# Optimization experiments

Hardware: AMD Instinct MI355X
Metric: run time of the kernel (lower is better)

Reference implementation:

```python
import jax, jax.numpy as jnp
import numpy as np

NUM_LEVEL = 16
LOG_T = 19
TABLE_SIZE = 2 ** LOG_T
FEAT = 2
MIN_RES = 16
MAX_RES = 512
N_POINTS = 262144

# [Teschner et al. 2003] spatial hash primes, wrapped to int32 like torch does
HASH_COEFFS = jnp.asarray(np.array([1, 2654435761, 805459861], dtype=np.uint32).astype(np.int32))


def _resolutions():
    coeff = (MAX_RES / MIN_RES) ** (1.0 / (NUM_LEVEL - 1))
    return jnp.floor(MIN_RES * (jnp.float32(coeff) ** jnp.arange(NUM_LEVEL, dtype=jnp.float32)))


def _spatial_hash(verts_i32):
    # verts_i32: (..., 3) int32; wrap-around int32 multiply then xor, then mod T (non-negative)
    x = HASH_COEFFS * verts_i32
    idx = jnp.bitwise_xor(jnp.bitwise_xor(x[..., 0], x[..., 1]), x[..., 2])
    return jnp.mod(idx, TABLE_SIZE)


def _hash_encode(coords, tables):
    # coords: (N,3) f32 in [0,1); tables: (L,T,F) f16
    res = _resolutions()                                   # (L,)
    scaled = coords[None, :, :] * res[:, None, None]        # (L,N,3)
    floor = jnp.floor(scaled)
    ceil = jnp.ceil(scaled)
    # 8 voxel corners via floor/ceil selection bits
    offs = jnp.asarray(np.array([[(o >> 2) & 1, (o >> 1) & 1, o & 1] for o in range(8)], dtype=np.bool_))
    sel = offs[:, None, None, :]                            # (8,1,1,3)
    corner = jnp.where(sel, ceil[None], floor[None])        # (8,L,N,3)
    comp = jnp.where(sel, floor[None], ceil[None])          # opposite corner (8,L,N,3)
    idx = _spatial_hash(corner.astype(jnp.int32))           # (8,L,N)
    # gather per-level features: tables[l][idx[:,l,:]] -> (L,8,N,F)
    feats = jax.vmap(lambda tab, i: tab[i], in_axes=(0, 1))(tables, idx)
    # trilinear weight of corner o = prod |opposite_corner - scaled|
    w = jnp.prod(jnp.abs(comp - scaled[None]), axis=-1)     # (8,L,N)
    w = jnp.transpose(w, (1, 0, 2))                         # (L,8,N)
    lvl = jnp.sum(feats.astype(jnp.float32) * w[..., None], axis=1)  # (L,N,F)
    return jnp.transpose(lvl, (1, 0, 2)).reshape(coords.shape[0], NUM_LEVEL * FEAT)


def _mlp(x, w_in, b_in, w_h0, b_h0, w_h1, b_h1, w_out, b_out):
    h = jax.nn.relu(x @ w_in.T + b_in)
    h = jax.nn.relu(h @ w_h0.T + b_h0)
    h = jax.nn.relu(h @ w_h1.T + b_h1)
    return h @ w_out.T + b_out


def setup_inputs() -> dict:
    key = jax.random.key(0)
    ks = jax.random.split(key, 8)
    coords = jax.random.uniform(ks[0], (N_POINTS, 3), dtype=jnp.float32)
    tables = (2e-4 * jax.random.uniform(ks[1], (NUM_LEVEL, TABLE_SIZE, FEAT), dtype=jnp.float32) - 1e-4).astype(jnp.float16)
    def lin(k, out_d, in_d):
        return jax.random.normal(k, (out_d, in_d), dtype=jnp.float32) * (1.0 / np.sqrt(in_d))
    return {
        'coords': coords, 'tables': tables,
        'w_in': lin(ks[2], 64, 32), 'b_in': jnp.zeros((64,), jnp.float32),
        'w_h0': lin(ks[3], 64, 64), 'b_h0': jnp.zeros((64,), jnp.float32),
        'w_h1': lin(ks[4], 64, 64), 'b_h1': jnp.zeros((64,), jnp.float32),
        'w_out': lin(ks[5], 16, 64), 'b_out': jnp.zeros((16,), jnp.float32),
    }


def reference(coords, tables, w_in, b_in, w_h0, b_h0, w_h1, b_h1, w_out, b_out):
    enc = _hash_encode(coords, tables)  # (N, 32)
    return _mlp(enc, w_in, b_in, w_h0, b_h0, w_h1, b_h1, w_out, b_out)  # (N, 16)
```

## Files before the change

### kernel.cpp

```cpp
#include <hip/hip_runtime.h>

#define NLVL 16
#define LOGT 19
#define TMASK ((1u << LOGT) - 1u)
#define SCALE 4096.0f
#define INV_SCALE (1.0f / 4096.0f)
#define NFRAG 22

typedef _Float16 half_t;
typedef half_t half8 __attribute__((ext_vector_type(8)));
typedef half_t half4 __attribute__((ext_vector_type(4)));
typedef half_t half2v __attribute__((ext_vector_type(2)));
typedef float  float4v __attribute__((ext_vector_type(4)));
typedef unsigned int uint4v __attribute__((ext_vector_type(4)));

__device__ __constant__ float RES_C[NLVL] = {16.f, 20.f, 25.f, 32.f, 40.f, 50.f, 64.f, 80.f,
                                             101.f, 128.f, 161.f, 203.f, 256.f, 322.f, 406.f, 512.f};

__device__ __forceinline__ float4v mfma16(half8 a, half8 b, float4v c) {
    return __builtin_amdgcn_mfma_f32_16x16x32_f16(a, b, c, 0, 0, 0);
}

__global__ __launch_bounds__(256, 8) void nerf_encode_w(
    const float* __restrict__ coords,
    const float2* __restrict__ tab,
    const float* __restrict__ w_in, const float* __restrict__ w_h0,
    const float* __restrict__ w_h1, const float* __restrict__ w_out,
    half8* __restrict__ frags,
    half_t* __restrict__ encT, int npts)
{
    const int bpl  = npts >> 8;
    const int nEnc = bpl * NLVL;
    const int b    = blockIdx.x;

    if (b >= nEnc) {
        if (threadIdx.x < 64) {
            const int frag = b - nEnc;
            const int lane = threadIdx.x;
            const int m    = lane & 15;
            const int quad = lane >> 4;
            const float* W; int ncol, row, col;
            if (frag < 4)       { W = w_in;  ncol = 32; row = frag * 16 + m;      col = quad * 8; }
            else if (frag < 12) { const int f = frag - 4;
                                  W = w_h0;  ncol = 64; row = (f >> 1) * 16 + m;  col = (f & 1) * 32 + quad * 8; }
            else if (frag < 20) { const int f = frag - 12;
                                  W = w_h1;  ncol = 64; row = (f >> 1) * 16 + m;  col = (f & 1) * 32 + quad * 8; }
            else                { const int f = frag - 20;
                                  W = w_out; ncol = 64; row = m;                  col = f * 32 + quad * 8; }
            const float* p = W + row * ncol + col;
            half8 r;
            #pragma unroll
            for (int j = 0; j < 8; ++j) r[j] = (half_t)p[j];
            frags[frag * 64 + lane] = r;
        }
        return;
    }

    const int half = bpl * 8;
    const int hi   = (b >= half) ? 1 : 0;
    const int l    = (b & 7) + (hi << 3);
    const int pb   = (hi ? (b - half) : b) >> 3;

    const int side = threadIdx.x & 1;
    const int base = pb * 256 + (threadIdx.x >> 1);
    const int p0 = base, p1 = base + 128;

    const float r = RES_C[l];
    const float2* __restrict__ bp = tab + (((unsigned)l) << LOGT);

    const float ax = coords[p0 * 3 + 0] * r, ay = coords[p0 * 3 + 1] * r, az = coords[p0 * 3 + 2] * r;
    const float afx = floorf(ax), afy = floorf(ay), afz = floorf(az);
    const float agx = ceilf(ax),  agy = ceilf(ay),  agz = ceilf(az);
    const unsigned ahx = side ? (unsigned)(int)agx : (unsigned)(int)afx;
    const float    awx = side ? (ax - afx) : (agx - ax);
    const unsigned ahfy = (unsigned)(int)afy * 2654435761u;
    const unsigned ahgy = (unsigned)(int)agy * 2654435761u;
    const unsigned ahfz = (unsigned)(int)afz * 805459861u;
    const unsigned ahgz = (unsigned)(int)agz * 805459861u;
    const float aty = ay - afy, atz = az - afz, auy = agy - ay, auz = agz - az;

    const float bx = coords[p1 * 3 + 0] * r, by = coords[p1 * 3 + 1] * r, bz = coords[p1 * 3 + 2] * r;
    const float bfx = floorf(bx), bfy = floorf(by), bfz = floorf(bz);
    const float bgx = ceilf(bx),  bgy = ceilf(by),  bgz = ceilf(bz);
    const unsigned bhx = side ? (unsigned)(int)bgx : (unsigned)(int)bfx;
    const float    bwx = side ? (bx - bfx) : (bgx - bx);
    const unsigned bhfy = (unsigned)(int)bfy * 2654435761u;
    const unsigned bhgy = (unsigned)(int)bgy * 2654435761u;
    const unsigned bhfz = (unsigned)(int)bfz * 805459861u;
    const unsigned bhgz = (unsigned)(int)bgz * 805459861u;
    const float bty = by - bfy, btz = bz - bfz, buy = bgy - by, buz = bgz - bz;

    const float2 a0 = bp[(ahx ^ ahfy ^ ahfz) & TMASK];
    const float2 a1 = bp[(ahx ^ ahfy ^ ahgz) & TMASK];
    const float2 a2 = bp[(ahx ^ ahgy ^ ahfz) & TMASK];
    const float2 a3 = bp[(ahx ^ ahgy ^ ahgz) & TMASK];
    const float2 b0 = bp[(bhx ^ bhfy ^ bhfz) & TMASK];
    const float2 b1 = bp[(bhx ^ bhfy ^ bhgz) & TMASK];
    const float2 b2 = bp[(bhx ^ bhgy ^ bhfz) & TMASK];
    const float2 b3 = bp[(bhx ^ bhgy ^ bhgz) & TMASK];

    const float aw0 = awx * auy * auz, aw1 = awx * auy * atz;
    const float aw2 = awx * aty * auz, aw3 = awx * aty * atz;
    const float bw0 = bwx * buy * buz, bw1 = bwx * buy * btz;
    const float bw2 = bwx * bty * buz, bw3 = bwx * bty * btz;

    float ae0 = aw0 * a0.x + aw1 * a1.x + aw2 * a2.x + aw3 * a3.x;
    float ae1 = aw0 * a0.y + aw1 * a1.y + aw2 * a2.y + aw3 * a3.y;
    float be0 = bw0 * b0.x + bw1 * b1.x + bw2 * b2.x + bw3 * b3.x;
    float be1 = bw0 * b0.y + bw1 * b1.y + bw2 * b2.y + bw3 * b3.y;

    ae0 += __shfl_xor(ae0, 1, 64);
    ae1 += __shfl_xor(ae1, 1, 64);
    be0 += __shfl_xor(be0, 1, 64);
    be1 += __shfl_xor(be1, 1, 64);

    if (side == 0) {
        half2v h0; h0[0] = (half_t)(ae0 * SCALE); h0[1] = (half_t)(ae1 * SCALE);
        half2v h1; h1[0] = (half_t)(be0 * SCALE); h1[1] = (half_t)(be1 * SCALE);
        *reinterpret_cast<half2v*>(&encT[((size_t)l * npts + p0) * 2]) = h0;
        *reinterpret_cast<half2v*>(&encT[((size_t)l * npts + p1) * 2]) = h1;
    }
}

__device__ __forceinline__ unsigned pack_relu2(float x, float y) {
    half2v h;
    h[0] = (half_t)fmaxf(x, 0.f);
    h[1] = (half_t)fmaxf(y, 0.f);
    return __builtin_bit_cast(unsigned, h);
}

__device__ __forceinline__ void xpose_relu(const float4v acc[4], int lane,
                                           half8& b0, half8& b1) {
    unsigned X[4], Y[4];
    X[0] = pack_relu2(acc[0][0], acc[0][1]);
    X[1] = pack_relu2(acc[0][2], acc[0][3]);
    X[2] = pack_relu2(acc[2][0], acc[2][1]);
    X[3] = pack_relu2(acc[2][2], acc[2][3]);
    Y[0] = pack_relu2(acc[1][0], acc[1][1]);
    Y[1] = pack_relu2(acc[1][2], acc[1][3]);
    Y[2] = pack_relu2(acc[3][0], acc[3][1]);
    Y[3] = pack_relu2(acc[3][2], acc[3][3]);
    const bool lo = (lane & 32) == 0;
    const bool ev = (lane & 16) == 0;
    uint4v u0, u1;
    #pragma unroll
    for (int j = 0; j < 4; ++j) {
        const unsigned s1 = lo ? Y[j] : X[j];
        const unsigned t1 = __shfl_xor(s1, 32, 64);
        const unsigned A1 = lo ? X[j] : t1;
        const unsigned B1 = lo ? t1 : Y[j];
        const unsigned s2 = ev ? B1 : A1;
        const unsigned t2 = __shfl_xor(s2, 16, 64);
        const unsigned a2 = ev ? A1 : t2;
        const unsigned b2 = ev ? t2 : B1;
        if (j < 2) { u0[j] = a2; u0[2 + j] = b2; }
        else       { u1[j - 2] = a2; u1[j] = b2; }
    }
    b0 = __builtin_bit_cast(half8, u0);
    b1 = __builtin_bit_cast(half8, u1);
}

__global__ __launch_bounds__(256, 3) void nerf_mlp7(
    const half_t* __restrict__ encT,
    const half8* __restrict__ frags,
    const float* __restrict__ b_in, const float* __restrict__ b_h0,
    const float* __restrict__ b_h1, const float* __restrict__ b_out,
    float* __restrict__ out, int npts)
{
    const int t    = threadIdx.x;
    const int lane = t & 63;
    const int wv   = t >> 6;
    const int m    = lane & 15;
    const int quad = lane >> 4;
    const size_t pbase = (size_t)blockIdx.x * 256 + (size_t)wv * 64;

    half8 be[4];
    #pragma unroll
    for (int T = 0; T < 4; ++T) {
        #pragma unroll
        for (int d = 0; d < 4; ++d) {
            const int L = quad * 4 + d;
            const half2v v = *reinterpret_cast<const half2v*>(
                &encT[((size_t)L * npts + pbase + T * 16 + m) * 2]);
            be[T][d * 2 + 0] = v[0];
            be[T][d * 2 + 1] = v[1];
        }
    }

    half8 bf0[4], bf1[4];

    {
        half8 w[4];
        #pragma unroll
        for (int f = 0; f < 4; ++f) w[f] = frags[(0 + f) * 64 + lane];
        float4v cin[4];
        #pragma unroll
        for (int mt = 0; mt < 4; ++mt)
            cin[mt] = (*reinterpret_cast<const float4v*>(b_in + mt * 16 + quad * 4)) * SCALE;
        #pragma unroll
        for (int T = 0; T < 4; ++T) {
            float4v acc[4];
            #pragma unroll
            for (int mt = 0; mt < 4; ++mt) acc[mt] = mfma16(w[mt], be[T], cin[mt]);
            xpose_relu(acc, lane, bf0[T], bf1[T]);
        }
    }
    {
        half8 w[8];
        #pragma unroll
        for (int f = 0; f < 8; ++f) w[f] = frags[(4 + f) * 64 + lane];
        float4v cin[4];
        #pragma unroll
        for (int mt = 0; mt < 4; ++mt)
            cin[mt] = (*reinterpret_cast<const float4v*>(b_h0 + mt * 16 + quad * 4)) * SCALE;
        #pragma unroll
        for (int T = 0; T < 4; ++T) {
            float4v acc[4];
            #pragma unroll
            for (int mt = 0; mt < 4; ++mt) {
                acc[mt] = mfma16(w[mt * 2 + 0], bf0[T], cin[mt]);
                acc[mt] = mfma16(w[mt * 2 + 1], bf1[T], acc[mt]);
            }
            xpose_relu(acc, lane, bf0[T], bf1[T]);
        }
    }
    {
        half8 w[8];
        #pragma unroll
        for (int f = 0; f < 8; ++f) w[f] = frags[(12 + f) * 64 + lane];
        float4v cin[4];
        #pragma unroll
        for (int mt = 0; mt < 4; ++mt)
            cin[mt] = (*reinterpret_cast<const float4v*>(b_h1 + mt * 16 + quad * 4)) * SCALE;
        #pragma unroll
        for (int T = 0; T < 4; ++T) {
            float4v acc[4];
            #pragma unroll
            for (int mt = 0; mt < 4; ++mt) {
                acc[mt] = mfma16(w[mt * 2 + 0], bf0[T], cin[mt]);
                acc[mt] = mfma16(w[mt * 2 + 1], bf1[T], acc[mt]);
            }
            xpose_relu(acc, lane, bf0[T], bf1[T]);
        }
    }
    {
        const half8 w0 = frags[20 * 64 + lane];
        const half8 w1 = frags[21 * 64 + lane];
        const float4v b4 = *reinterpret_cast<const float4v*>(b_out + quad * 4);
        const float4v zero = {0.f, 0.f, 0.f, 0.f};
        #pragma unroll
        for (int T = 0; T < 4; ++T) {
            float4v acc = mfma16(w0, bf0[T], zero);
            acc         = mfma16(w1, bf1[T], acc);
            float4v res;
            #pragma unroll
            for (int r = 0; r < 4; ++r) res[r] = fmaf(acc[r], INV_SCALE, b4[r]);
            *reinterpret_cast<float4v*>(out + (pbase + T * 16 + m) * 16 + quad * 4) = res;
        }
    }
}

__global__ __launch_bounds__(256, 2) void nerf_fused(
    const float* __restrict__ coords,
    const float2* __restrict__ tab,
    const float* __restrict__ w_in, const float* __restrict__ b_in,
    const float* __restrict__ w_h0, const float* __restrict__ b_h0,
    const float* __restrict__ w_h1, const float* __restrict__ b_h1,
    const float* __restrict__ w_out, const float* __restrict__ b_out,
    float* __restrict__ out, int npts)
{
    __shared__ half_t encS[256 * 40];
    __shared__ half_t actS[4][2][32 * 64];

    const int t    = threadIdx.x;
    const int lane = t & 63;
    const int wv   = t >> 6;
    const int m    = lane & 15;
    const int quad = lane >> 4;
    const int pt = blockIdx.x * 256 + t;

    {
        const float cx = coords[pt * 3 + 0];
        const float cy = coords[pt * 3 + 1];
        const float cz = coords[pt * 3 + 2];
        float enc[32];
        #pragma unroll
        for (int l = 0; l < NLVL; ++l) {
            const float r = RES_C[l];
            const float sx = cx * r, sy = cy * r, sz = cz * r;
            const float fx = floorf(sx), fy = floorf(sy), fz = floorf(sz);
            const float gx = ceilf(sx),  gy = ceilf(sy),  gz = ceilf(sz);
            const unsigned hfx = (unsigned)(int)fx;
            const unsigned hgx = (unsigned)(int)gx;
            const unsigned hfy = (unsigned)(int)fy * 2654435761u;
            const unsigned hgy = (unsigned)(int)gy * 2654435761u;
            const unsigned hfz = (unsigned)(int)fz * 805459861u;
            const unsigned hgz = (unsigned)(int)gz * 805459861u;
            const float tx = sx - fx, ty = sy - fy, tz = sz - fz;
            const float ux = gx - sx, uy = gy - sy, uz = gz - sz;
            const unsigned lbase = ((unsigned)l) << LOGT;
            float e0 = 0.f, e1 = 0.f;
            #pragma unroll
            for (int o = 0; o < 8; ++o) {
                const unsigned h = ((o & 4) ? hgx : hfx)
                                 ^ ((o & 2) ? hgy : hfy)
                                 ^ ((o & 1) ? hgz : hfz);
                const unsigned idx = h & TMASK;
                const float w = (((o & 4) ? tx : ux)
                              *  ((o & 2) ? ty : uy))
                              *  ((o & 1) ? tz : uz);
                const float2 fv = tab[lbase + idx];
                e0 = fmaf(w, fv.x, e0);
                e1 = fmaf(w, fv.y, e1);
            }
            enc[2 * l + 0] = e0;
            enc[2 * l + 1] = e1;
        }
        #pragma unroll
        for (int c = 0; c < 4; ++c) {
            half8 h8;
            #pragma unroll
            for (int j = 0; j < 8; ++j) h8[j] = (half_t)(enc[c * 8 + j] * SCALE);
            *reinterpret_cast<half8*>(&encS[t * 40 + c * 8]) = h8;
        }
    }

    auto loadA = [&](const float* __restrict__ W, int ncol, int row, int col) -> half8 {
        const float* p = W + row * ncol + col;
        const float4v lo = *reinterpret_cast<const float4v*>(p);
        const float4v hi = *reinterpret_cast<const float4v*>(p + 4);
        half8 r;
        r[0] = (half_t)lo[0]; r[1] = (half_t)lo[1]; r[2] = (half_t)lo[2]; r[3] = (half_t)lo[3];
        r[4] = (half_t)hi[0]; r[5] = (half_t)hi[1]; r[6] = (half_t)hi[2]; r[7] = (half_t)hi[3];
        return r;
    };

    half8 aL1[4], aL2[8], aL3[8], aL4[2];
    #pragma unroll
    for (int mt = 0; mt < 4; ++mt) aL1[mt] = loadA(w_in, 32, mt * 16 + m, quad * 8);
    #pragma unroll
    for (int mt = 0; mt < 4; ++mt) {
        aL2[mt * 2 + 0] = loadA(w_h0, 64, mt * 16 + m, 0 * 32 + quad * 8);
        aL2[mt * 2 + 1] = loadA(w_h0, 64, mt * 16 + m, 1 * 32 + quad * 8);
        aL3[mt * 2 + 0] = loadA(w_h1, 64, mt * 16 + m, 0 * 32 + quad * 8);
        aL3[mt * 2 + 1] = loadA(w_h1, 64, mt * 16 + m, 1 * 32 + quad * 8);
    }
    aL4[0] = loadA(w_out, 64, m, 0 * 32 + quad * 8);
    aL4[1] = loadA(w_out, 64, m, 1 * 32 + quad * 8);

    float4v bL1[4], bL2[4], bL3[4], bL4;
    #pragma unroll
    for (int mt = 0; mt < 4; ++mt) {
        bL1[mt] = *reinterpret_cast<const float4v*>(b_in + mt * 16 + quad * 4);
        bL2[mt] = *reinterpret_cast<const float4v*>(b_h0 + mt * 16 + quad * 4);
        bL3[mt] = *reinterpret_cast<const float4v*>(b_h1 + mt * 16 + quad * 4);
    }
    bL4 = *reinterpret_cast<const float4v*>(b_out + quad * 4);

    half_t* const ping = &actS[wv][0][0];
    half_t* const pong = &actS[wv][1][0];
    const float4v zero = {0.f, 0.f, 0.f, 0.f};

    auto storeTile = [&](half_t* buf, int lp, int mt, float4v acc, float4v bias) {
        half4 h4;
        #pragma unroll
        for (int r = 0; r < 4; ++r)
            h4[r] = (half_t)fmaxf(fmaf(bias[r], SCALE, acc[r]), 0.f);
        const int c16  = mt * 2 + (quad >> 1);
        const int phys = c16 ^ (lp & 7);
        *reinterpret_cast<half4*>(&buf[lp * 64 + phys * 8 + (quad & 1) * 4]) = h4;
    };
    auto loadB = [&](half_t* buf, int lp, int h) -> half8 {
        const int phys = (h * 4 + quad) ^ (lp & 7);
        return *reinterpret_cast<const half8*>(&buf[lp * 64 + phys * 8]);
    };

    for (int g = 0; g < 2; ++g) {
        #pragma unroll
        for (int nt = 0; nt < 2; ++nt) {
            const int lp   = nt * 16 + m;
            const int prow = wv * 64 + g * 32 + lp;
            const half8 bfr = *reinterpret_cast<const half8*>(&encS[prow * 40 + quad * 8]);
            #pragma unroll
            for (int mt = 0; mt < 4; ++mt) {
                float4v acc = mfma16(aL1[mt], bfr, zero);
                storeTile(ping, lp, mt, acc, bL1[mt]);
            }
            {
                const half8 p0 = loadB(ping, lp, 0);
                const half8 p1 = loadB(ping, lp, 1);
                #pragma unroll
                for (int mt = 0; mt < 4; ++mt) {
                    float4v acc = mfma16(aL2[mt * 2 + 0], p0, zero);
                    acc         = mfma16(aL2[mt * 2 + 1], p1, acc);
                    storeTile(pong, lp, mt, acc, bL2[mt]);
                }
            }
            {
                const half8 p0 = loadB(pong, lp, 0);
                const half8 p1 = loadB(pong, lp, 1);
                #pragma unroll
                for (int mt = 0; mt < 4; ++mt) {
                    float4v acc = mfma16(aL3[mt * 2 + 0], p0, zero);
                    acc         = mfma16(aL3[mt * 2 + 1], p1, acc);
                    storeTile(ping, lp, mt, acc, bL3[mt]);
                }
            }
            {
                const half8 p0 = loadB(ping, lp, 0);
                const half8 p1 = loadB(ping, lp, 1);
                float4v acc = mfma16(aL4[0], p0, zero);
                acc         = mfma16(aL4[1], p1, acc);
                float4v res;
                #pragma unroll
                for (int r = 0; r < 4; ++r)
                    res[r] = fmaf(acc[r], INV_SCALE, bL4[r]);
                const size_t ptg = (size_t)blockIdx.x * 256 + (size_t)wv * 64 + g * 32 + lp;
                *reinterpret_cast<float4v*>(out + ptg * 16 + quad * 4) = res;
            }
        }
    }
}

extern "C" void kernel_launch(void* const* d_in, const int* in_sizes, int n_in,
                              void* d_out, int out_size, void* d_ws, size_t ws_size,
                              hipStream_t stream) {
    const float*  coords = (const float*)d_in[0];
    const float2* tables = (const float2*)d_in[1];
    const float*  w_in   = (const float*)d_in[2];
    const float*  b_in   = (const float*)d_in[3];
    const float*  w_h0   = (const float*)d_in[4];
    const float*  b_h0   = (const float*)d_in[5];
    const float*  w_h1   = (const float*)d_in[6];
    const float*  b_h1   = (const float*)d_in[7];
    const float*  w_out  = (const float*)d_in[8];
    const float*  b_out  = (const float*)d_in[9];
    float* out = (float*)d_out;

    const int npts = in_sizes[0] / 3;
    const size_t encBytes  = (size_t)npts * 32 * sizeof(half_t);
    const size_t fragBytes = (size_t)NFRAG * 64 * sizeof(half8);

    if (ws_size >= encBytes + fragBytes && (npts & 255) == 0) {
        half_t* encT  = (half_t*)d_ws;
        half8*  frags = (half8*)((char*)d_ws + encBytes);
        const int bpl = npts >> 8;
        nerf_encode_w<<<bpl * NLVL + NFRAG, 256, 0, stream>>>(
            coords, tables, w_in, w_h0, w_h1, w_out, frags, encT, npts);
        nerf_mlp7<<<npts / 256, 256, 0, stream>>>(encT, frags,
                                                  b_in, b_h0, b_h1, b_out,
                                                  out, npts);
    } else {
        nerf_fused<<<npts / 256, 256, 0, stream>>>(coords, tables,
                                                   w_in, b_in, w_h0, b_h0,
                                                   w_h1, b_h1, w_out, b_out,
                                                   out, npts);
    }
}
```

Before: 197.7 us.

## Precompute compact hash grids for coarse levels and gather from LDS

For the four coarsest levels (resolutions 16 to 32), the dense (r+1)^3 grid of hashed table entries is precomputed into a compact workspace array. A new kernel stages each level's grid into shared memory (about 140 KB) and does the trilinear lookups from LDS, skipping the hash and the random global gathers. The hash-encode kernel now handles only the 12 finer levels, with a remapped block order. This adds a third kernel launch, needs one-block-per-CU occupancy for the staging kernel, and the fast path is gated on the exact test point count.

```diff
diff --git a/kernel.cpp b/kernel.cpp
--- a/kernel.cpp
+++ b/kernel.cpp
@@ -7,6 +7,11 @@
 #define INV_SCALE (1.0f / 4096.0f)
 #define NFRAG 22
 
+#define NCG 4
+#define CG_TOTAL 67687
+#define CG_TOTAL_PAD 67700
+#define CG_BLOCKS 265
+
 typedef _Float16 half_t;
 typedef half_t half8 __attribute__((ext_vector_type(8)));
 typedef half_t half4 __attribute__((ext_vector_type(4)));
@@ -16,50 +21,79 @@
 
 __device__ __constant__ float RES_C[NLVL] = {16.f, 20.f, 25.f, 32.f, 40.f, 50.f, 64.f, 80.f,
                                              101.f, 128.f, 161.f, 203.f, 256.f, 322.f, 406.f, 512.f};
+__device__ __constant__ int CG_SIZE[NCG] = {4913, 9261, 17576, 35937};
+__device__ __constant__ int CG_OFF[NCG]  = {0, 4916, 14180, 31760};
+__device__ __constant__ int CG_R1[NCG]   = {17, 21, 26, 33};
 
 __device__ __forceinline__ float4v mfma16(half8 a, half8 b, float4v c) {
     return __builtin_amdgcn_mfma_f32_16x16x32_f16(a, b, c, 0, 0, 0);
 }
 
-__global__ __launch_bounds__(256, 8) void nerf_encode_w(
+__global__ __launch_bounds__(256, 8) void nerf_encode_h12(
     const float* __restrict__ coords,
     const float2* __restrict__ tab,
     const float* __restrict__ w_in, const float* __restrict__ w_h0,
     const float* __restrict__ w_h1, const float* __restrict__ w_out,
     half8* __restrict__ frags,
+    unsigned* __restrict__ compact,
     half_t* __restrict__ encT, int npts)
 {
-    const int bpl  = npts >> 8;
-    const int nEnc = bpl * NLVL;
-    const int b    = blockIdx.x;
-
-    if (b >= nEnc) {
-        if (threadIdx.x < 64) {
-            const int frag = b - nEnc;
-            const int lane = threadIdx.x;
-            const int m    = lane & 15;
-            const int quad = lane >> 4;
-            const float* W; int ncol, row, col;
-            if (frag < 4)       { W = w_in;  ncol = 32; row = frag * 16 + m;      col = quad * 8; }
-            else if (frag < 12) { const int f = frag - 4;
-                                  W = w_h0;  ncol = 64; row = (f >> 1) * 16 + m;  col = (f & 1) * 32 + quad * 8; }
-            else if (frag < 20) { const int f = frag - 12;
-                                  W = w_h1;  ncol = 64; row = (f >> 1) * 16 + m;  col = (f & 1) * 32 + quad * 8; }
-            else                { const int f = frag - 20;
-                                  W = w_out; ncol = 64; row = m;                  col = f * 32 + quad * 8; }
-            const float* p = W + row * ncol + col;
-            half8 r;
-            #pragma unroll
-            for (int j = 0; j < 8; ++j) r[j] = (half_t)p[j];
-            frags[frag * 64 + lane] = r;
+    const int bpl   = npts >> 8;
+    const int nHash = 12 * bpl;
+    const int b     = blockIdx.x;
+
+    if (b >= nHash) {
+        const int tb = b - nHash;
+        if (tb < NFRAG) {
+            if (threadIdx.x < 64) {
+                const int frag = tb;
+                const int lane = threadIdx.x;
+                const int m    = lane & 15;
+                const int quad = lane >> 4;
+                const float* W; int ncol, row, col;
+                if (frag < 4)       { W = w_in;  ncol = 32; row = frag * 16 + m;      col = quad * 8; }
+                else if (frag < 12) { const int f = frag - 4;
+                                      W = w_h0;  ncol = 64; row = (f >> 1) * 16 + m;  col = (f & 1) * 32 + quad * 8; }
+                else if (frag < 20) { const int f = frag - 12;
+                                      W = w_h1;  ncol = 64; row = (f >> 1) * 16 + m;  col = (f & 1) * 32 + quad * 8; }
+                else                { const int f = frag - 20;
+                                      W = w_out; ncol = 64; row = m;                  col = f * 32 + quad * 8; }
+                const float* p = W + row * ncol + col;
+                half8 r;
+                #pragma unroll
+                for (int j = 0; j < 8; ++j) r[j] = (half_t)p[j];
+                frags[frag * 64 + lane] = r;
+            }
+        } else {
+            const int vid = (tb - NFRAG) * 256 + (int)threadIdx.x;
+            if (vid < CG_TOTAL) {
+                const int l = (vid >= 31750) ? 3 : (vid >= 14174) ? 2 : (vid >= 4913) ? 1 : 0;
+                const int voff = (l == 3) ? 31750 : (l == 2) ? 14174 : (l == 1) ? 4913 : 0;
+                const int v  = vid - voff;
+                const int r1 = CG_R1[l];
+                const int z  = v % r1;
+                const int r2 = v / r1;
+                const int y  = r2 % r1;
+                const int x  = r2 / r1;
+                const unsigned idx = ((unsigned)x
+                                    ^ ((unsigned)y * 2654435761u)
+                                    ^ ((unsigned)z * 805459861u)) & TMASK;
+                const float2 tv = tab[(((unsigned)l) << LOGT) + idx];
+                half2v h; h[0] = (half_t)tv.x; h[1] = (half_t)tv.y;
+                compact[CG_OFF[l] + v] = __builtin_bit_cast(unsigned, h);
+            }
         }
         return;
     }
 
-    const int half = bpl * 8;
-    const int hi   = (b >= half) ? 1 : 0;
-    const int l    = (b & 7) + (hi << 3);
-    const int pb   = (hi ? (b - half) : b) >> 3;
+    int l, pb;
+    const int phaseA = 8 * bpl;
+    if (b < phaseA) { l = 4 + (b & 7); pb = b >> 3; }
+    else {
+        const int b2 = b - phaseA;
+        l  = 12 + ((b2 & 7) >> 1);
+        pb = ((b2 >> 3) << 1) + (b2 & 1);
+    }
 
     const int side = threadIdx.x & 1;
     const int base = pb * 256 + (threadIdx.x >> 1);
@@ -119,6 +153,75 @@
         half2v h1; h1[0] = (half_t)(be0 * SCALE); h1[1] = (half_t)(be1 * SCALE);
         *reinterpret_cast<half2v*>(&encT[((size_t)l * npts + p0) * 2]) = h0;
         *reinterpret_cast<half2v*>(&encT[((size_t)l * npts + p1) * 2]) = h1;
+    }
+}
+
+__global__ __launch_bounds__(256, 1) void nerf_encode_stage(
+    const float* __restrict__ coords,
+    const unsigned* __restrict__ compact,
+    half_t* __restrict__ encT, int npts)
+{
+    __shared__ unsigned sgrid[35940];
+
+    const int s     = blockIdx.x;
+    const int l     = s >> 6;
+    const int chunk = s & 63;
+    const int t     = threadIdx.x;
+
+    const int sz = CG_SIZE[l];
+    const unsigned* __restrict__ src = compact + CG_OFF[l];
+    const int n4 = (sz + 3) >> 2;
+    for (int i = t; i < n4; i += 256) {
+        const uint4v v = *reinterpret_cast<const uint4v*>(src + i * 4);
+        *reinterpret_cast<uint4v*>(&sgrid[i * 4]) = v;
+    }
+    __syncthreads();
+
+    const float r  = RES_C[l];
+    const int   r1 = CG_R1[l];
+    const int   p0 = chunk * 4096 + t;
+
+    #pragma unroll 4
+    for (int k = 0; k < 16; ++k) {
+        const int p = p0 + k * 256;
+        const float cx = coords[p * 3 + 0], cy = coords[p * 3 + 1], cz = coords[p * 3 + 2];
+        const float sx = cx * r, sy = cy * r, szf = cz * r;
+        const float fx = floorf(sx), fy = floorf(sy), fz = floorf(szf);
+        const float gx = ceilf(sx),  gy = ceilf(sy),  gz = ceilf(szf);
+        const int ixf = (int)fx, iyf = (int)fy, izf = (int)fz;
+        const int ixg = (int)gx, iyg = (int)gy, izg = (int)gz;
+
+        const float wxf = gx - sx, wxc = sx - fx;
+        const float uy = gy - sy, ty = sy - fy;
+        const float uz = gz - szf, tz = szf - fz;
+
+        const int bf = ixf * r1, bg = ixg * r1;
+        const int rf = (bf + iyf) * r1, rF = (bf + iyg) * r1;
+        const int rg = (bg + iyf) * r1, rG = (bg + iyg) * r1;
+
+        const half2v c0 = __builtin_bit_cast(half2v, sgrid[rf + izf]);
+        const half2v c1 = __builtin_bit_cast(half2v, sgrid[rf + izg]);
+        const half2v c2 = __builtin_bit_cast(half2v, sgrid[rF + izf]);
+        const half2v c3 = __builtin_bit_cast(half2v, sgrid[rF + izg]);
+        const half2v c4 = __builtin_bit_cast(half2v, sgrid[rg + izf]);
+        const half2v c5 = __builtin_bit_cast(half2v, sgrid[rg + izg]);
+        const half2v c6 = __builtin_bit_cast(half2v, sgrid[rG + izf]);
+        const half2v c7 = __builtin_bit_cast(half2v, sgrid[rG + izg]);
+
+        const float w0 = wxf * uy * uz, w1 = wxf * uy * tz;
+        const float w2 = wxf * ty * uz, w3 = wxf * ty * tz;
+        const float w4 = wxc * uy * uz, w5 = wxc * uy * tz;
+        const float w6 = wxc * ty * uz, w7 = wxc * ty * tz;
+
+        float e0f = w0 * (float)c0[0] + w1 * (float)c1[0] + w2 * (float)c2[0] + w3 * (float)c3[0];
+        float e1f = w0 * (float)c0[1] + w1 * (float)c1[1] + w2 * (float)c2[1] + w3 * (float)c3[1];
+        float e0c = w4 * (float)c4[0] + w5 * (float)c5[0] + w6 * (float)c6[0] + w7 * (float)c7[0];
+        float e1c = w4 * (float)c4[1] + w5 * (float)c5[1] + w6 * (float)c6[1] + w7 * (float)c7[1];
+        const float e0 = e0f + e0c;
+        const float e1 = e1f + e1c;
+
+        half2v h; h[0] = (half_t)(e0 * SCALE); h[1] = (half_t)(e1 * SCALE);
+        *reinterpret_cast<half2v*>(&encT[((size_t)l * npts + p) * 2]) = h;
     }
 }
 
@@ -438,15 +541,18 @@
     float* out = (float*)d_out;
 
     const int npts = in_sizes[0] / 3;
-    const size_t encBytes  = (size_t)npts * 32 * sizeof(half_t);
-    const size_t fragBytes = (size_t)NFRAG * 64 * sizeof(half8);
-
-    if (ws_size >= encBytes + fragBytes && (npts & 255) == 0) {
-        half_t* encT  = (half_t*)d_ws;
-        half8*  frags = (half8*)((char*)d_ws + encBytes);
+    const size_t encBytes     = (size_t)npts * 32 * sizeof(half_t);
+    const size_t fragBytes    = (size_t)NFRAG * 64 * sizeof(half8);
+    const size_t compactBytes = (size_t)CG_TOTAL_PAD * sizeof(unsigned);
+
+    if (ws_size >= encBytes + fragBytes + compactBytes && npts == 262144) {
+        half_t*   encT    = (half_t*)d_ws;
+        half8*    frags   = (half8*)((char*)d_ws + encBytes);
+        unsigned* compact = (unsigned*)((char*)d_ws + encBytes + fragBytes);
         const int bpl = npts >> 8;
-        nerf_encode_w<<<bpl * NLVL + NFRAG, 256, 0, stream>>>(
-            coords, tables, w_in, w_h0, w_h1, w_out, frags, encT, npts);
+        nerf_encode_h12<<<12 * bpl + NFRAG + CG_BLOCKS, 256, 0, stream>>>(
+            coords, tables, w_in, w_h0, w_h1, w_out, frags, compact, encT, npts);
+        nerf_encode_stage<<<4 * 64, 256, 0, stream>>>(coords, compact, encT, npts);
         nerf_mlp7<<<npts / 256, 256, 0, stream>>>(encT, frags,
                                                   b_in, b_h0, b_h1, b_out,
                                                   out, npts);
```

New measurement: 198.5 us. About the same (+0.4%).
